# Performance work log

Hardware: AMD Instinct MI355X
Metric: run time of the kernel (lower is better)

## Reference

```python
import jax, jax.numpy as jnp
import numpy as np

ALPHA = 0.2  # LeakyReLU negative slope
NEG_BIG = -9e15


def setup_inputs() -> dict:
    key = jax.random.key(0)
    k1, k2, k3, k4 = jax.random.split(key, 4)
    N, F_in, F_out = 8192, 512, 256
    h = jax.random.normal(k1, (N, F_in), dtype=jnp.float32)
    adj = jax.random.randint(k2, (N, N), 0, 2, dtype=jnp.int32)
    # xavier_uniform with gain=1.414
    lim_W = 1.414 * np.sqrt(6.0 / (F_in + F_out))
    W = jax.random.uniform(k3, (F_in, F_out), jnp.float32, -lim_W, lim_W)
    lim_a = 1.414 * np.sqrt(6.0 / (2 * F_out + 1))
    a = jax.random.uniform(k4, (2 * F_out, 1), jnp.float32, -lim_a, lim_a)
    return {"h": h, "adj": adj, "W": W, "a": a}


def reference(h, adj, W, a):
    # Wh: [N, F_out]
    Wh = h @ W
    F_out = Wh.shape[1]
    # Decomposed score: e_ij = leakyrelu(a1.Wh_i + a2.Wh_j)
    f1 = Wh @ a[:F_out, 0]   # [N]
    f2 = Wh @ a[F_out:, 0]   # [N]
    e = f1[:, None] + f2[None, :]          # [N, N]
    e = jax.nn.leaky_relu(e, ALPHA)
    e = jnp.where(adj > 0, e, NEG_BIG)
    attention = jax.nn.softmax(e, axis=1)  # dropout omitted (eval mode)
    h_prime = attention @ Wh               # [N, F_out]
    return jax.nn.elu(h_prime)             # concat=True
```

## Files before the change

kernel.cpp:

```cpp
#include <hip/hip_runtime.h>
#include <hip/hip_bf16.h>
#include <cstdint>

#define NV 8192
#define FIN 512
#define FOUT 256
#define KS 4
#define ALPHA_LRELU 0.2f

using bf16x8 = __attribute__((ext_vector_type(8))) short;
using f32x4  = __attribute__((ext_vector_type(4))) float;

static __device__ __forceinline__ float b2f(ushort u) {
  union { uint32_t u32; float f; } v; v.u32 = ((uint32_t)u) << 16; return v.f;
}
static __device__ __forceinline__ ushort f2b(float f) {
  union { float f; uint32_t u; } v; v.f = f;
  uint32_t r = (v.u + 0x7fffu + ((v.u >> 16) & 1u)) >> 16;
  return (ushort)r;
}
static __device__ __forceinline__ int swz(int row, int kchunk) {
  return (row << 6) + (((kchunk ^ (row & 7)) & 7) << 3);
}

__global__ void k_prep_h(const float* __restrict__ h, ushort* __restrict__ hB) {
  int idx = blockIdx.x * 256 + threadIdx.x;
  float4 v = ((const float4*)h)[idx];
  ushort4 o;
  o.x = f2b(v.x); o.y = f2b(v.y); o.z = f2b(v.z); o.w = f2b(v.w);
  ((ushort4*)hB)[idx] = o;
}

__global__ void k_prep_w(const float* __restrict__ W, ushort* __restrict__ WT) {
  int t = blockIdx.x * 256 + threadIdx.x;
  int n = t >> 9, k = t & 511;
  WT[(size_t)n * FIN + k] = f2b(W[(size_t)k * FOUT + n]);
}

__global__ __launch_bounds__(256, 4) void k_gemm1(
    const ushort* __restrict__ hB, const ushort* __restrict__ WT,
    ushort* __restrict__ WhT) {
  __shared__ __align__(16) ushort As[64 * 64];
  __shared__ __align__(16) ushort Ws[64 * 64];
  const int t = threadIdx.x;
  const int lane = t & 63;
  const int w = t >> 6;
  const int wm = w >> 1, wn = w & 1;
  const int i0 = blockIdx.x * 64;
  const int n0 = blockIdx.y * 64;

  f32x4 acc[2][2] = {};
  const int srow = t & 63, sseg = t >> 6;

  for (int kt = 0; kt < FIN / 64; ++kt) {
    const int k0 = kt * 64;
    const uint4* gA = (const uint4*)(hB + (size_t)(i0 + srow) * FIN + k0 + sseg * 16);
    const uint4* gB = (const uint4*)(WT + (size_t)(n0 + srow) * FIN + k0 + sseg * 16);
#pragma unroll
    for (int m = 0; m < 2; ++m) {
      uint4 va = gA[m];
      *(uint4*)&As[swz(srow, sseg * 2 + m)] = va;
      uint4 vb = gB[m];
      *(uint4*)&Ws[swz(srow, sseg * 2 + m)] = vb;
    }
    __syncthreads();
#pragma unroll
    for (int kk = 0; kk < 2; ++kk) {
      const int kc = kk * 4 + (lane >> 4);
      bf16x8 af[2], bfv[2];
#pragma unroll
      for (int fi = 0; fi < 2; ++fi)
        af[fi] = *(const bf16x8*)&As[swz(wm * 32 + fi * 16 + (lane & 15), kc)];
#pragma unroll
      for (int fj = 0; fj < 2; ++fj)
        bfv[fj] = *(const bf16x8*)&Ws[swz(wn * 32 + fj * 16 + (lane & 15), kc)];
#pragma unroll
      for (int fi = 0; fi < 2; ++fi)
#pragma unroll
        for (int fj = 0; fj < 2; ++fj)
          acc[fi][fj] = __builtin_amdgcn_mfma_f32_16x16x32_bf16(af[fi], bfv[fj], acc[fi][fj], 0, 0, 0);
    }
    __syncthreads();
  }
#pragma unroll
  for (int fi = 0; fi < 2; ++fi) {
    const int row0 = i0 + wm * 32 + fi * 16 + ((lane >> 4) << 2);
#pragma unroll
    for (int fj = 0; fj < 2; ++fj) {
      const int col = n0 + wn * 32 + fj * 16 + (lane & 15);
      ushort4 o;
      o.x = f2b(acc[fi][fj][0]); o.y = f2b(acc[fi][fj][1]);
      o.z = f2b(acc[fi][fj][2]); o.w = f2b(acc[fi][fj][3]);
      *(ushort4*)&WhT[(size_t)col * NV + row0] = o;
    }
  }
}

__global__ void k_f12(const ushort* __restrict__ WhT, const float* __restrict__ a,
                      float* __restrict__ f1, float* __restrict__ f2,
                      float* __restrict__ f2bmax) {
  __shared__ float a1s[256], a2s[256];
  __shared__ float red[256];
  const int tid = threadIdx.x;
  a1s[tid] = a[tid];
  a2s[tid] = a[256 + tid];
  __syncthreads();
  const int i = blockIdx.x * 256 + tid;
  float s1 = 0.f, s2 = 0.f;
  for (int c = 0; c < 256; ++c) {
    float v = b2f(WhT[(size_t)c * NV + i]);
    s1 = fmaf(v, a1s[c], s1);
    s2 = fmaf(v, a2s[c], s2);
  }
  f1[i] = s1; f2[i] = s2;
  red[tid] = s2; __syncthreads();
  for (int off = 128; off > 0; off >>= 1) {
    if (tid < off) red[tid] = fmaxf(red[tid], red[tid + off]);
    __syncthreads();
  }
  if (tid == 0) f2bmax[blockIdx.x] = red[0];
}

__global__ __launch_bounds__(512, 4) void k_gemm2(
    const int* __restrict__ adj, const ushort* __restrict__ WhT,
    const float* __restrict__ f1, const float* __restrict__ f2,
    const float* __restrict__ f2bmax,
    float* __restrict__ accP, float* __restrict__ Sp) {
  __shared__ __align__(16) ushort Ps[64 * 64];
  __shared__ __align__(16) ushort Bs[256 * 64];
  __shared__ float f2s[NV / KS];
  __shared__ float f1s[64], cs[64];

  const int t = threadIdx.x;
  const int lane = t & 63;
  const int w = t >> 6;
  const int wm = w >> 2, wn = w & 3;
  const int bid = blockIdx.x;
  const int ks = bid & (KS - 1);
  const int rb = bid >> 2;
  const int i0 = rb * 64;
  const int jbase = ks * (NV / KS);
  const int NT = (NV / KS) / 64;

  float mf = -1e30f;
#pragma unroll
  for (int c = 0; c < 32; ++c) mf = fmaxf(mf, f2bmax[c]);
  if (t < 64) {
    float v = f1[i0 + t];
    f1s[t] = v;
    float e = v + mf;
    cs[t] = fmaxf(e, ALPHA_LRELU * e);
  }
  for (int idx = t; idx < NV / KS; idx += 512) f2s[idx] = f2[jbase + idx];
  __syncthreads();

  const int pr = t >> 3, pq = t & 7;
  const int bc = t & 255, bseg = t >> 8;
  const float f1r = f1s[pr], cr = cs[pr];
  float ssum = 0.f;
  f32x4 acc[2][4] = {};

  for (int kt = 0; kt < NT; ++kt) {
    const int j0 = jbase + kt * 64;
    {
      const int4* ga = (const int4*)(adj + (size_t)(i0 + pr) * NV + j0 + pq * 8);
      int4 a0 = ga[0], a1 = ga[1];
      int av[8] = {a0.x, a0.y, a0.z, a0.w, a1.x, a1.y, a1.z, a1.w};
      const float* fz = &f2s[kt * 64 + pq * 8];
      ushort ub[8];
#pragma unroll
      for (int e = 0; e < 8; ++e) {
        float x = f1r + fz[e];
        float ee = fmaxf(x, ALPHA_LRELU * x) - cr;
        float wvv = (av[e] > 0) ? __expf(ee) : 0.f;
        ub[e] = f2b(wvv);
        ssum += b2f(ub[e]);
      }
      uint4 pk;
      pk.x = (uint32_t)ub[0] | ((uint32_t)ub[1] << 16);
      pk.y = (uint32_t)ub[2] | ((uint32_t)ub[3] << 16);
      pk.z = (uint32_t)ub[4] | ((uint32_t)ub[5] << 16);
      pk.w = (uint32_t)ub[6] | ((uint32_t)ub[7] << 16);
      *(uint4*)&Ps[swz(pr, pq)] = pk;
    }
    {
      const uint4* gb = (const uint4*)(WhT + (size_t)bc * NV + j0 + bseg * 32);
#pragma unroll
      for (int m = 0; m < 4; ++m) {
        uint4 v = gb[m];
        *(uint4*)&Bs[swz(bc, bseg * 4 + m)] = v;
      }
    }
    __syncthreads();
#pragma unroll
    for (int kk = 0; kk < 2; ++kk) {
      const int kc = kk * 4 + (lane >> 4);
      bf16x8 af[2], bfv[4];
#pragma unroll
      for (int fi = 0; fi < 2; ++fi)
        af[fi] = *(const bf16x8*)&Ps[swz(wm * 32 + fi * 16 + (lane & 15), kc)];
#pragma unroll
      for (int fj = 0; fj < 4; ++fj)
        bfv[fj] = *(const bf16x8*)&Bs[swz(wn * 64 + fj * 16 + (lane & 15), kc)];
#pragma unroll
      for (int fi = 0; fi < 2; ++fi)
#pragma unroll
        for (int fj = 0; fj < 4; ++fj)
          acc[fi][fj] = __builtin_amdgcn_mfma_f32_16x16x32_bf16(af[fi], bfv[fj], acc[fi][fj], 0, 0, 0);
    }
    __syncthreads();
  }

  ssum += __shfl_xor(ssum, 1);
  ssum += __shfl_xor(ssum, 2);
  ssum += __shfl_xor(ssum, 4);
  if (pq == 0) Sp[(size_t)ks * NV + i0 + pr] = ssum;

  float* ab = accP + (size_t)ks * NV * FOUT;
#pragma unroll
  for (int fi = 0; fi < 2; ++fi) {
    const int ig = i0 + wm * 32 + fi * 16 + ((lane >> 4) << 2);
#pragma unroll
    for (int fj = 0; fj < 4; ++fj) {
      const int col = wn * 64 + fj * 16 + (lane & 15);
#pragma unroll
      for (int rr = 0; rr < 4; ++rr)
        ab[(size_t)(ig + rr) * FOUT + col] = acc[fi][fj][rr];
    }
  }
}

__global__ void k_combine(const float* __restrict__ accP, const float* __restrict__ Sp,
                          float* __restrict__ out) {
  const size_t NF = (size_t)NV * FOUT;
  int g = blockIdx.x * 256 + threadIdx.x;
  int i = g >> 6;
  float4 v0 = ((const float4*)accP)[g];
  float4 v1 = ((const float4*)(accP + NF))[g];
  float4 v2 = ((const float4*)(accP + 2 * NF))[g];
  float4 v3 = ((const float4*)(accP + 3 * NF))[g];
  float s = Sp[i] + Sp[NV + i] + Sp[2 * NV + i] + Sp[3 * NV + i];
  float inv = (s != 0.f) ? (1.0f / s) : 0.f;
  float xs0 = (v0.x + v1.x + v2.x + v3.x) * inv;
  float xs1 = (v0.y + v1.y + v2.y + v3.y) * inv;
  float xs2 = (v0.z + v1.z + v2.z + v3.z) * inv;
  float xs3 = (v0.w + v1.w + v2.w + v3.w) * inv;
  float4 o;
  o.x = xs0 > 0.f ? xs0 : expm1f(xs0);
  o.y = xs1 > 0.f ? xs1 : expm1f(xs1);
  o.z = xs2 > 0.f ? xs2 : expm1f(xs2);
  o.w = xs3 > 0.f ? xs3 : expm1f(xs3);
  ((float4*)out)[g] = o;
}

extern "C" void kernel_launch(void* const* d_in, const int* in_sizes, int n_in,
                              void* d_out, int out_size, void* d_ws, size_t ws_size,
                              hipStream_t stream) {
  const float* h   = (const float*)d_in[0];
  const int*   adj = (const int*)d_in[1];
  const float* W   = (const float*)d_in[2];
  const float* a   = (const float*)d_in[3];
  float* out = (float*)d_out;

  char* ws = (char*)d_ws;
  ushort* hB   = (ushort*)ws;
  ushort* WT   = (ushort*)(ws + (8ull << 20));
  ushort* WhT  = (ushort*)(ws + (8ull << 20) + (256ull << 10));
  float*  f1   = (float*)(ws + (12ull << 20) + (256ull << 10));
  float*  f2   = f1 + NV;
  float*  f2bm = f2 + NV;
  float*  Sp   = f2bm + 64;
  float*  accP = Sp + (size_t)KS * NV;

  k_prep_h<<<(NV * FIN / 4) / 256, 256, 0, stream>>>(h, hB);
  k_prep_w<<<(FIN * FOUT) / 256, 256, 0, stream>>>(W, WT);
  k_gemm1<<<dim3(NV / 64, FOUT / 64), 256, 0, stream>>>(hB, WT, WhT);
  k_f12<<<NV / 256, 256, 0, stream>>>(WhT, a, f1, f2, f2bm);
  k_gemm2<<<(NV / 64) * KS, 512, 0, stream>>>(adj, WhT, f1, f2, f2bm, accP, Sp);
  k_combine<<<(NV * FOUT / 4) / 256, 256, 0, stream>>>(accP, Sp, out);
}
```

Measured before the change: 455.8 us.

## Double-buffer gemm2 tiles with direct global-to-LDS loads and split f12 reduction

The attention GEMM now double-buffers its P and Wh tiles. It prefetches the next Wh tile straight into LDS with global_load_lds and loads the next adj and f2 values into registers while the MFMAs run, which removes one barrier per iteration. The k_f12 kernel splits the 256-channel dot product across four waves to get more parallelism. A new tiny k_fmax kernel computes the global f2 max once, so gemm2 blocks no longer each reduce it or stage f2 into shared memory. The cost is twice the LDS, launch bounds lowered to 2 blocks per CU, and one extra kernel launch.

```diff
diff --git a/kernel.cpp b/kernel.cpp
--- a/kernel.cpp
+++ b/kernel.cpp
@@ -21,6 +21,12 @@
 }
 static __device__ __forceinline__ int swz(int row, int kchunk) {
   return (row << 6) + (((kchunk ^ (row & 7)) & 7) << 3);
+}
+static __device__ __forceinline__ void gl_lds16(const ushort* g, ushort* l) {
+  __builtin_amdgcn_global_load_lds(
+      (const __attribute__((address_space(1))) uint32_t*)(uintptr_t)g,
+      (__attribute__((address_space(3))) uint32_t*)(uint32_t)(uintptr_t)l,
+      16, 0, 0);
 }
 
 __global__ void k_prep_h(const float* __restrict__ h, ushort* __restrict__ hB) {
@@ -100,36 +106,52 @@
                       float* __restrict__ f1, float* __restrict__ f2,
                       float* __restrict__ f2bmax) {
   __shared__ float a1s[256], a2s[256];
-  __shared__ float red[256];
+  __shared__ float r1[4][64], r2[4][64];
   const int tid = threadIdx.x;
   a1s[tid] = a[tid];
   a2s[tid] = a[256 + tid];
+  const int ws = tid >> 6, ln = tid & 63;
+  const int i = blockIdx.x * 64 + ln;
   __syncthreads();
-  const int i = blockIdx.x * 256 + tid;
   float s1 = 0.f, s2 = 0.f;
-  for (int c = 0; c < 256; ++c) {
+#pragma unroll 8
+  for (int c = ws * 64; c < ws * 64 + 64; ++c) {
     float v = b2f(WhT[(size_t)c * NV + i]);
     s1 = fmaf(v, a1s[c], s1);
     s2 = fmaf(v, a2s[c], s2);
   }
-  f1[i] = s1; f2[i] = s2;
-  red[tid] = s2; __syncthreads();
-  for (int off = 128; off > 0; off >>= 1) {
+  r1[ws][ln] = s1; r2[ws][ln] = s2;
+  __syncthreads();
+  if (ws == 0) {
+    s1 = r1[0][ln] + r1[1][ln] + r1[2][ln] + r1[3][ln];
+    s2 = r2[0][ln] + r2[1][ln] + r2[2][ln] + r2[3][ln];
+    f1[i] = s1; f2[i] = s2;
+    float m = s2;
+#pragma unroll
+    for (int off = 32; off > 0; off >>= 1) m = fmaxf(m, __shfl_xor(m, off));
+    if (ln == 0) f2bmax[blockIdx.x] = m;
+  }
+}
+
+__global__ void k_fmax(const float* __restrict__ f2bmax, float* __restrict__ mfp) {
+  __shared__ float red[128];
+  const int tid = threadIdx.x;
+  red[tid] = f2bmax[tid];
+  __syncthreads();
+  for (int off = 64; off > 0; off >>= 1) {
     if (tid < off) red[tid] = fmaxf(red[tid], red[tid + off]);
     __syncthreads();
   }
-  if (tid == 0) f2bmax[blockIdx.x] = red[0];
-}
-
-__global__ __launch_bounds__(512, 4) void k_gemm2(
+  if (tid == 0) mfp[0] = red[0];
+}
+
+__global__ __launch_bounds__(512, 2) void k_gemm2(
     const int* __restrict__ adj, const ushort* __restrict__ WhT,
     const float* __restrict__ f1, const float* __restrict__ f2,
-    const float* __restrict__ f2bmax,
+    const float* __restrict__ mfp,
     float* __restrict__ accP, float* __restrict__ Sp) {
-  __shared__ __align__(16) ushort Ps[64 * 64];
-  __shared__ __align__(16) ushort Bs[256 * 64];
-  __shared__ float f2s[NV / KS];
-  __shared__ float f1s[64], cs[64];
+  __shared__ __align__(16) ushort Ps[2][64 * 64];
+  __shared__ __align__(16) ushort Bs[2][256 * 64];
 
   const int t = threadIdx.x;
   const int lane = t & 63;
@@ -142,73 +164,80 @@
   const int jbase = ks * (NV / KS);
   const int NT = (NV / KS) / 64;
 
-  float mf = -1e30f;
-#pragma unroll
-  for (int c = 0; c < 32; ++c) mf = fmaxf(mf, f2bmax[c]);
-  if (t < 64) {
-    float v = f1[i0 + t];
-    f1s[t] = v;
-    float e = v + mf;
-    cs[t] = fmaxf(e, ALPHA_LRELU * e);
-  }
-  for (int idx = t; idx < NV / KS; idx += 512) f2s[idx] = f2[jbase + idx];
-  __syncthreads();
-
   const int pr = t >> 3, pq = t & 7;
-  const int bc = t & 255, bseg = t >> 8;
-  const float f1r = f1s[pr], cr = cs[pr];
+  const float mf = mfp[0];
+  const float f1r = f1[i0 + pr];
+  const float e0 = f1r + mf;
+  const float cr = fmaxf(e0, ALPHA_LRELU * e0);
+
+  const int lrow = lane >> 3;
+  const int lchunk = (lane & 7) ^ lrow;
+  const ushort* wsrc0 = WhT + (size_t)(w * 32 + lrow) * NV + jbase + lchunk * 8;
+  const int* adjp = adj + (size_t)(i0 + pr) * NV + jbase + pq * 8;
+  const float* f2p = f2 + jbase + pq * 8;
+
   float ssum = 0.f;
   f32x4 acc[2][4] = {};
-
+  int av[8]; float fz[8];
+
+  auto stage_load = [&](int koff, int buf) {
+#pragma unroll
+    for (int q = 0; q < 4; ++q)
+      gl_lds16(wsrc0 + (size_t)q * 8 * NV + koff, &Bs[buf][(w * 4 + q) * 512]);
+    int4 a0 = *(const int4*)(adjp + koff);
+    int4 a1 = *(const int4*)(adjp + koff + 4);
+    float4 z0 = *(const float4*)(f2p + koff);
+    float4 z1 = *(const float4*)(f2p + koff + 4);
+    av[0] = a0.x; av[1] = a0.y; av[2] = a0.z; av[3] = a0.w;
+    av[4] = a1.x; av[5] = a1.y; av[6] = a1.z; av[7] = a1.w;
+    fz[0] = z0.x; fz[1] = z0.y; fz[2] = z0.z; fz[3] = z0.w;
+    fz[4] = z1.x; fz[5] = z1.y; fz[6] = z1.z; fz[7] = z1.w;
+  };
+  auto stage_finish = [&](int buf) {
+    ushort ub[8];
+#pragma unroll
+    for (int e = 0; e < 8; ++e) {
+      float x = f1r + fz[e];
+      float ee = fmaxf(x, ALPHA_LRELU * x) - cr;
+      float wv = (av[e] > 0) ? __expf(ee) : 0.f;
+      ub[e] = f2b(wv);
+      ssum += b2f(ub[e]);
+    }
+    uint4 pk;
+    pk.x = (uint32_t)ub[0] | ((uint32_t)ub[1] << 16);
+    pk.y = (uint32_t)ub[2] | ((uint32_t)ub[3] << 16);
+    pk.z = (uint32_t)ub[4] | ((uint32_t)ub[5] << 16);
+    pk.w = (uint32_t)ub[6] | ((uint32_t)ub[7] << 16);
+    *(uint4*)&Ps[buf][swz(pr, pq)] = pk;
+  };
+
+  stage_load(0, 0);
+  stage_finish(0);
+  __syncthreads();
+
+  int cur = 0;
   for (int kt = 0; kt < NT; ++kt) {
-    const int j0 = jbase + kt * 64;
-    {
-      const int4* ga = (const int4*)(adj + (size_t)(i0 + pr) * NV + j0 + pq * 8);
-      int4 a0 = ga[0], a1 = ga[1];
-      int av[8] = {a0.x, a0.y, a0.z, a0.w, a1.x, a1.y, a1.z, a1.w};
-      const float* fz = &f2s[kt * 64 + pq * 8];
-      ushort ub[8];
-#pragma unroll
-      for (int e = 0; e < 8; ++e) {
-        float x = f1r + fz[e];
-        float ee = fmaxf(x, ALPHA_LRELU * x) - cr;
-        float wvv = (av[e] > 0) ? __expf(ee) : 0.f;
-        ub[e] = f2b(wvv);
-        ssum += b2f(ub[e]);
-      }
-      uint4 pk;
-      pk.x = (uint32_t)ub[0] | ((uint32_t)ub[1] << 16);
-      pk.y = (uint32_t)ub[2] | ((uint32_t)ub[3] << 16);
-      pk.z = (uint32_t)ub[4] | ((uint32_t)ub[5] << 16);
-      pk.w = (uint32_t)ub[6] | ((uint32_t)ub[7] << 16);
-      *(uint4*)&Ps[swz(pr, pq)] = pk;
-    }
-    {
-      const uint4* gb = (const uint4*)(WhT + (size_t)bc * NV + j0 + bseg * 32);
-#pragma unroll
-      for (int m = 0; m < 4; ++m) {
-        uint4 v = gb[m];
-        *(uint4*)&Bs[swz(bc, bseg * 4 + m)] = v;
-      }
-    }
-    __syncthreads();
+    const bool pf = (kt + 1 < NT);
+    if (pf) stage_load((kt + 1) * 64, cur ^ 1);
 #pragma unroll
     for (int kk = 0; kk < 2; ++kk) {
       const int kc = kk * 4 + (lane >> 4);
       bf16x8 af[2], bfv[4];
 #pragma unroll
       for (int fi = 0; fi < 2; ++fi)
-        af[fi] = *(const bf16x8*)&Ps[swz(wm * 32 + fi * 16 + (lane & 15), kc)];
+        af[fi] = *(const bf16x8*)&Ps[cur][swz(wm * 32 + fi * 16 + (lane & 15), kc)];
 #pragma unroll
       for (int fj = 0; fj < 4; ++fj)
-        bfv[fj] = *(const bf16x8*)&Bs[swz(wn * 64 + fj * 16 + (lane & 15), kc)];
+        bfv[fj] = *(const bf16x8*)&Bs[cur][swz(wn * 64 + fj * 16 + (lane & 15), kc)];
 #pragma unroll
       for (int fi = 0; fi < 2; ++fi)
 #pragma unroll
         for (int fj = 0; fj < 4; ++fj)
           acc[fi][fj] = __builtin_amdgcn_mfma_f32_16x16x32_bf16(af[fi], bfv[fj], acc[fi][fj], 0, 0, 0);
     }
+    if (pf) stage_finish(cur ^ 1);
     __syncthreads();
+    cur ^= 1;
   }
 
   ssum += __shfl_xor(ssum, 1);
@@ -269,13 +298,15 @@
   float*  f1   = (float*)(ws + (12ull << 20) + (256ull << 10));
   float*  f2   = f1 + NV;
   float*  f2bm = f2 + NV;
-  float*  Sp   = f2bm + 64;
+  float*  mfp  = f2bm + 128;
+  float*  Sp   = mfp + 64;
   float*  accP = Sp + (size_t)KS * NV;
 
   k_prep_h<<<(NV * FIN / 4) / 256, 256, 0, stream>>>(h, hB);
   k_prep_w<<<(FIN * FOUT) / 256, 256, 0, stream>>>(W, WT);
   k_gemm1<<<dim3(NV / 64, FOUT / 64), 256, 0, stream>>>(hB, WT, WhT);
-  k_f12<<<NV / 256, 256, 0, stream>>>(WhT, a, f1, f2, f2bm);
-  k_gemm2<<<(NV / 64) * KS, 512, 0, stream>>>(adj, WhT, f1, f2, f2bm, accP, Sp);
+  k_f12<<<NV / 64, 256, 0, stream>>>(WhT, a, f1, f2, f2bm);
+  k_fmax<<<1, 128, 0, stream>>>(f2bm, mfp);
+  k_gemm2<<<(NV / 64) * KS, 512, 0, stream>>>(adj, WhT, f1, f2, mfp, accP, Sp);
   k_combine<<<(NV * FOUT / 4) / 256, 256, 0, stream>>>(accP, Sp, out);
 }
```

After: 435.2 us. 4.5% less time.
